# Kernel tuning notes

Hardware: AMD Instinct MI355X
Metric: run time of the kernel (lower is better)

Reference implementation:

```python
import jax, jax.numpy as jnp
import numpy as np

EMBED = 768
HEADS = 12
HEAD_DIM = EMBED // HEADS
WINDOW_SIZES = (16, 64, 256)
LN_EPS = 1e-5


def setup_inputs() -> dict:
    key = jax.random.key(0)
    ks = jax.random.split(key, 8)
    B, S = 4, 1024
    s = 1.0 / np.sqrt(EMBED)
    return {
        "query": jax.random.normal(ks[0], (B, S, EMBED), dtype=jnp.float32),
        "key": jax.random.normal(ks[1], (B, S, EMBED), dtype=jnp.float32),
        "value": jax.random.normal(ks[2], (B, S, EMBED), dtype=jnp.float32),
        "attention_mask": jnp.ones((B, S), dtype=jnp.float32),
        "Wq": jax.random.normal(ks[3], (EMBED, EMBED), dtype=jnp.float32) * s,
        "bq": jnp.zeros((EMBED,), dtype=jnp.float32),
        "Wk": jax.random.normal(ks[4], (EMBED, EMBED), dtype=jnp.float32) * s,
        "bk": jnp.zeros((EMBED,), dtype=jnp.float32),
        "Wv": jax.random.normal(ks[5], (EMBED, EMBED), dtype=jnp.float32) * s,
        "bv": jnp.zeros((EMBED,), dtype=jnp.float32),
        "window_weights": jnp.ones((len(WINDOW_SIZES),), dtype=jnp.float32) / len(WINDOW_SIZES),
        "gamma": jnp.ones((EMBED,), dtype=jnp.float32),
        "beta": jnp.zeros((EMBED,), dtype=jnp.float32),
    }


def reference(query, key, value, attention_mask, Wq, bq, Wk, bk, Wv, bv,
              window_weights, gamma, beta):
    B, S, _ = query.shape

    def proj(x, W, b):
        # [B,S,E] -> [B,H,S,D]  (torch nn.Linear: x @ W.T + b)
        return (x @ W.T + b).reshape(B, S, HEADS, HEAD_DIM).transpose(0, 2, 1, 3)

    q = proj(query, Wq, bq)
    k = proj(key, Wk, bk)
    v = proj(value, Wv, bv)

    # full [B,H,S,S] scores (dropout in eval mode = identity)
    scores = jnp.einsum("bhqd,bhkd->bhqk", q, k) / np.sqrt(HEAD_DIM)

    idx = jnp.arange(S)
    am = attention_mask[:, None, None, :]  # broadcast over heads and query dim
    combined = jnp.zeros_like(scores)
    for i, w in enumerate(WINDOW_SIZES):
        # band mask |i-j| <= w; note scores are multiplicatively masked
        # and carried across scales, exactly as in the torch loop
        band = (jnp.abs(idx[:, None] - idx[None, :]) <= w).astype(scores.dtype)
        scores = scores * band * am
        combined = combined + window_weights[i] * jax.nn.softmax(scores, axis=-1)

    context = jnp.einsum("bhqk,bhkd->bhqd", combined, v)
    context = context.transpose(0, 2, 1, 3).reshape(B, S, EMBED)
    q_flat = q.transpose(0, 2, 1, 3).reshape(B, S, EMBED)

    x = q_flat + context
    mean = jnp.mean(x, axis=-1, keepdims=True)
    var = jnp.var(x, axis=-1, keepdims=True)
    return gamma * (x - mean) / jnp.sqrt(var + LN_EPS) + beta
```

## Files before the change

### kernel.cpp

```cpp
#include <hip/hip_runtime.h>
#include <hip/hip_bf16.h>

#define EMB   768
#define SEQ   1024
#define NBAT  4
#define MROWS 4096
#define NHEAD 12
#define HD    64
#define WIN   16
#define QB    16
#define KB    64
#define LN_EPS 1e-5f

typedef __attribute__((ext_vector_type(8))) short bf16x8;
typedef __attribute__((ext_vector_type(4))) float f32x4;
typedef unsigned short u16;
typedef unsigned int   u32;

static __device__ inline u16 f2bf(float f) {
    union { float f; u32 u; } a; a.f = f;
    u32 u = a.u;
    u32 r = (u + 0x7fffu + ((u >> 16) & 1u)) >> 16;
    return (u16)r;
}
static __device__ inline float bf2f(u16 x) {
    union { u32 u; float f; } c; c.u = ((u32)x) << 16; return c.f;
}

#define ACT4 786432u
#define WT4  147456u
__global__ __launch_bounds__(256) void cast_all(
    const float* __restrict__ q, const float* __restrict__ k, const float* __restrict__ v,
    const float* __restrict__ wq, const float* __restrict__ wk, const float* __restrict__ wv,
    u16* __restrict__ Abf, u16* __restrict__ Wbf, float* __restrict__ Vsum)
{
    u32 u = blockIdx.x * 256u + threadIdx.x;
    if (u < NBAT * EMB) Vsum[u] = 0.f;
    const float* src; u16* dst; u32 off;
    if (u < 3u * ACT4) {
        u32 which = u / ACT4;
        off = (u - which * ACT4) * 4u;
        src = which == 0 ? q : (which == 1 ? k : v);
        dst = Abf + (size_t)which * 3145728u + off;
    } else {
        u32 w2 = u - 3u * ACT4;
        u32 which = w2 / WT4;
        off = (w2 - which * WT4) * 4u;
        src = which == 0 ? wq : (which == 1 ? wk : wv);
        dst = Wbf + (size_t)which * 589824u + off;
    }
    float4 val = *(const float4*)(src + off);
    ushort4 o;
    o.x = f2bf(val.x); o.y = f2bf(val.y); o.z = f2bf(val.z); o.w = f2bf(val.w);
    *(ushort4*)dst = o;
}

#define GK 768
#define GN 768

static __device__ inline void gload_lds16(const void* g, void* l) {
    __builtin_amdgcn_global_load_lds((const __attribute__((address_space(1))) void*)g,
                                     (__attribute__((address_space(3))) void*)l, 16, 0, 0);
}

__global__ __launch_bounds__(256) void gemm_qkv(
    const u16* __restrict__ Abase, const u16* __restrict__ Wbase,
    const float* __restrict__ bq, const float* __restrict__ bk, const float* __restrict__ bv,
    u16* __restrict__ Qb, u16* __restrict__ Kb, u16* __restrict__ Vb,
    float* __restrict__ Vsum)
{
    const int z = blockIdx.z;
    const u16* A = Abase + (size_t)z * (MROWS * GK);
    const u16* W = Wbase + (size_t)z * (GN * GK);
    const float* bias = (z == 0) ? bq : ((z == 1) ? bk : bv);
    u16* Ob = (z == 0) ? Qb : ((z == 1) ? Kb : Vb);

    int id = blockIdx.y * 6 + blockIdx.x;
    int swz = (id & 7) * 48 + (id >> 3);
    const int bm = (swz / 6) * 64, bn = (swz % 6) * 128;

    const int tid = threadIdx.x, wave = tid >> 6, lane = tid & 63;

    __shared__ __align__(16) u16 As[2][64 * 64];
    __shared__ __align__(16) u16 Bs[2][128 * 64];

    f32x4 acc[2][4];
#pragma unroll
    for (int i = 0; i < 2; ++i)
#pragma unroll
        for (int j = 0; j < 4; ++j) acc[i][j] = (f32x4){0.f, 0.f, 0.f, 0.f};

    const int wr = (wave >> 1) * 32, wc = (wave & 1) * 64;
    const int r0 = lane & 15, hk = lane >> 4;

    int arow[2], acol[2], brow[4], bcol[4];
#pragma unroll
    for (int j = 0; j < 2; ++j) {
        int c = j * 256 + tid;
        arow[j] = c >> 3;
        acol[j] = ((c & 7) ^ (arow[j] & 7)) * 8;
    }
#pragma unroll
    for (int j = 0; j < 4; ++j) {
        int c = j * 256 + tid;
        brow[j] = c >> 3;
        bcol[j] = ((c & 7) ^ (brow[j] & 7)) * 8;
    }

#define GEMM_STAGE(buf, K0) do { \
    _Pragma("unroll") for (int j = 0; j < 2; ++j) \
        gload_lds16(A + (size_t)(bm + arow[j]) * GK + (K0) + acol[j], \
                    &As[buf][(j * 256 + tid) * 8]); \
    _Pragma("unroll") for (int j = 0; j < 4; ++j) \
        gload_lds16(W + (size_t)(bn + brow[j]) * GK + (K0) + bcol[j], \
                    &Bs[buf][(j * 256 + tid) * 8]); \
} while (0)

#define GEMM_COMPUTE(buf) do { \
    bf16x8 af[2][2], bg[2][4]; \
    _Pragma("unroll") for (int kk = 0; kk < 2; ++kk) { \
        _Pragma("unroll") for (int i = 0; i < 2; ++i) { \
            int ra = wr + i * 16 + r0; int sa = (kk * 4 + hk) ^ (ra & 7); \
            af[kk][i] = *(const bf16x8*)&As[buf][ra * 64 + sa * 8]; } \
        _Pragma("unroll") for (int j = 0; j < 4; ++j) { \
            int rb = wc + j * 16 + r0; int sb = (kk * 4 + hk) ^ (rb & 7); \
            bg[kk][j] = *(const bf16x8*)&Bs[buf][rb * 64 + sb * 8]; } } \
    _Pragma("unroll") for (int kk = 0; kk < 2; ++kk) \
    _Pragma("unroll") for (int i = 0; i < 2; ++i) \
    _Pragma("unroll") for (int j = 0; j < 4; ++j) \
        acc[i][j] = __builtin_amdgcn_mfma_f32_16x16x32_bf16(af[kk][i], bg[kk][j], acc[i][j], 0, 0, 0); \
} while (0)

    GEMM_STAGE(0, 0);
    for (int t = 0; t < 11; ++t) {
        int cur = t & 1;
        GEMM_STAGE(cur ^ 1, (t + 1) * 64);
        asm volatile("s_waitcnt vmcnt(6)" ::: "memory");
        __builtin_amdgcn_sched_barrier(0);
        __builtin_amdgcn_s_barrier();
        __builtin_amdgcn_sched_barrier(0);
        GEMM_COMPUTE(cur);
        __builtin_amdgcn_sched_barrier(0);
        __builtin_amdgcn_s_barrier();
        __builtin_amdgcn_sched_barrier(0);
    }
    asm volatile("s_waitcnt vmcnt(0)" ::: "memory");
    __builtin_amdgcn_sched_barrier(0);
    __builtin_amdgcn_s_barrier();
    __builtin_amdgcn_sched_barrier(0);
    GEMM_COMPUTE(1);

#undef GEMM_STAGE
#undef GEMM_COMPUTE

    const int cl = lane & 15, rb4 = (lane >> 4) * 4;
#pragma unroll
    for (int i = 0; i < 2; ++i)
#pragma unroll
        for (int j = 0; j < 4; ++j) {
            int col = bn + wc + j * 16 + cl;
            float b_ = bias[col];
#pragma unroll
            for (int r = 0; r < 4; ++r) {
                int row = bm + wr + i * 16 + rb4 + r;
                Ob[(size_t)row * GN + col] = f2bf(acc[i][j][r] + b_);
            }
        }

    if (z == 2) {
        const int bb = bm >> 10;
#pragma unroll
        for (int j = 0; j < 4; ++j) {
            int col = bn + wc + j * 16 + cl;
            float s = bias[col] * 8.f;
#pragma unroll
            for (int i = 0; i < 2; ++i)
#pragma unroll
                for (int r = 0; r < 4; ++r) s += acc[i][j][r];
            s += __shfl_xor(s, 16, 64);
            s += __shfl_xor(s, 32, 64);
            if (hk == 0)
                atomicAdd(&Vsum[bb * EMB + col], s);
        }
    }
}

__global__ __launch_bounds__(768, 3) void attn_ln(
    const u16* __restrict__ Qb, const u16* __restrict__ Kb, const u16* __restrict__ Vb,
    const float* __restrict__ Vsum, const float* __restrict__ am, const float* __restrict__ ww,
    const float* __restrict__ gamma, const float* __restrict__ beta, float* __restrict__ out)
{
    int id = blockIdx.x + 64 * blockIdx.y;
    int swz = (id & 7) * 32 + (id >> 3);
    const int qt = swz & 63, b = swz >> 6;

    const int q0 = qt * QB;
    int kstart = q0 - WIN;
    if (kstart < 0) kstart = 0;
    if (kstart > SEQ - KB) kstart = SEQ - KB;

    const int h = threadIdx.x >> 6, lane = threadIdx.x & 63;
    const int fr = lane & 15, hk = lane >> 4;
    const int kof = hk * 8, rowg = hk * 4;

    __shared__ __align__(16) u16 Ps[NHEAD][QB][68];
    __shared__ __align__(16) float xs[QB][772];
    __shared__ float ps1[QB][13], ps2[QB][13];
    __shared__ float mu[QB], rs[QB];

    const float w0 = ww[0], w1 = ww[1], w2 = ww[2];

    bf16x8 aq[2], bk4[4][2], bv4[4][2];
    {
        const u16* qb = Qb + ((size_t)(b * SEQ + q0)) * EMB + h * HD;
#pragma unroll
        for (int kk = 0; kk < 2; ++kk)
            aq[kk] = *(const bf16x8*)(qb + (size_t)fr * EMB + kk * 32 + kof);
        const u16* kb = Kb + ((size_t)(b * SEQ + kstart)) * EMB + h * HD;
#pragma unroll
        for (int nj = 0; nj < 4; ++nj)
#pragma unroll
            for (int kk = 0; kk < 2; ++kk)
                bk4[nj][kk] = *(const bf16x8*)(kb + (size_t)(nj * 16 + fr) * EMB + kk * 32 + kof);
        const u16* vb = Vb + ((size_t)(b * SEQ + kstart)) * EMB + h * HD;
#pragma unroll
        for (int nj = 0; nj < 4; ++nj)
#pragma unroll
            for (int kk = 0; kk < 2; ++kk) {
                union { bf16x8 v; u16 s[8]; } tmp;
#pragma unroll
                for (int j = 0; j < 8; ++j)
                    tmp.s[j] = vb[(size_t)(kk * 32 + kof + j) * EMB + nj * 16 + fr];
                bv4[nj][kk] = tmp.v;
            }
    }

    f32x4 sc[4];
#pragma unroll
    for (int j = 0; j < 4; ++j) sc[j] = (f32x4){0.f, 0.f, 0.f, 0.f};
#pragma unroll
    for (int kk = 0; kk < 2; ++kk)
#pragma unroll
        for (int nj = 0; nj < 4; ++nj)
            sc[nj] = __builtin_amdgcn_mfma_f32_16x16x32_bf16(aq[kk], bk4[nj][kk], sc[nj], 0, 0, 0);

    float amv[4];
#pragma unroll
    for (int nj = 0; nj < 4; ++nj) amv[nj] = am[b * SEQ + kstart + nj * 16 + fr];

    float t[4][4], cj[4][4], ua[4];
#pragma unroll
    for (int nj = 0; nj < 4; ++nj)
#pragma unroll
        for (int r = 0; r < 4; ++r) {
            int qrow = q0 + rowg + r;
            int kcol = kstart + nj * 16 + fr;
            int d = qrow - kcol; if (d < 0) d = -d;
            t[nj][r] = (d <= WIN) ? sc[nj][r] * 0.125f * amv[nj] : 0.f;
            cj[nj][r] = 0.f;
        }
#pragma unroll
    for (int r = 0; r < 4; ++r) ua[r] = 0.f;

#pragma unroll
    for (int it = 0; it < 3; ++it) {
        float wwi = it == 0 ? w0 : (it == 1 ? w1 : w2);
#pragma unroll
        for (int r = 0; r < 4; ++r) {
            float m = 0.f;
#pragma unroll
            for (int nj = 0; nj < 4; ++nj) m = fmaxf(m, t[nj][r]);
#pragma unroll
            for (int o = 1; o < 16; o <<= 1) m = fmaxf(m, __shfl_xor(m, o, 64));
            float e4[4], s = 0.f;
#pragma unroll
            for (int nj = 0; nj < 4; ++nj) { e4[nj] = __expf(t[nj][r] - m); s += e4[nj]; }
#pragma unroll
            for (int o = 1; o < 16; o <<= 1) s += __shfl_xor(s, o, 64);
            float un = __expf(-m);
            s += (float)(SEQ - KB) * un;
            float inv = wwi / s;
#pragma unroll
            for (int nj = 0; nj < 4; ++nj) cj[nj][r] += e4[nj] * inv;
            ua[r] += un * inv;
        }
        if (it < 2) {
#pragma unroll
            for (int nj = 0; nj < 4; ++nj)
#pragma unroll
                for (int r = 0; r < 4; ++r) t[nj][r] *= amv[nj];
        }
    }

#pragma unroll
    for (int nj = 0; nj < 4; ++nj)
#pragma unroll
        for (int r = 0; r < 4; ++r)
            Ps[h][rowg + r][nj * 16 + fr] = f2bf(cj[nj][r] - ua[r]);

    f32x4 pv[4];
#pragma unroll
    for (int j = 0; j < 4; ++j) pv[j] = (f32x4){0.f, 0.f, 0.f, 0.f};
#pragma unroll
    for (int kk = 0; kk < 2; ++kk) {
        bf16x8 ap = *(const bf16x8*)&Ps[h][fr][kk * 32 + kof];
#pragma unroll
        for (int nj = 0; nj < 4; ++nj)
            pv[nj] = __builtin_amdgcn_mfma_f32_16x16x32_bf16(ap, bv4[nj][kk], pv[nj], 0, 0, 0);
    }

    float vs[4];
#pragma unroll
    for (int nj = 0; nj < 4; ++nj) vs[nj] = Vsum[b * EMB + h * HD + nj * 16 + fr];

    float xv[4][4];
#pragma unroll
    for (int nj = 0; nj < 4; ++nj)
#pragma unroll
        for (int r = 0; r < 4; ++r) {
            int row = q0 + rowg + r;
            float qres = bf2f(Qb[((size_t)(b * SEQ + row)) * EMB + h * HD + nj * 16 + fr]);
            xv[nj][r] = qres + pv[nj][r] + ua[r] * vs[nj];
            xs[rowg + r][h * HD + nj * 16 + fr] = xv[nj][r];
        }

    float s1r[4], s2r[4];
#pragma unroll
    for (int r = 0; r < 4; ++r) {
        float a = 0.f, c = 0.f;
#pragma unroll
        for (int nj = 0; nj < 4; ++nj) { a += xv[nj][r]; c += xv[nj][r] * xv[nj][r]; }
#pragma unroll
        for (int o = 1; o < 16; o <<= 1) { a += __shfl_xor(a, o, 64); c += __shfl_xor(c, o, 64); }
        s1r[r] = a; s2r[r] = c;
    }
    if (fr == 0) {
#pragma unroll
        for (int r = 0; r < 4; ++r) { ps1[rowg + r][h] = s1r[r]; ps2[rowg + r][h] = s2r[r]; }
    }
    __syncthreads();
    if (h == 0 && lane < QB) {
        float a = 0.f, c = 0.f;
#pragma unroll
        for (int w = 0; w < NHEAD; ++w) { a += ps1[lane][w]; c += ps2[lane][w]; }
        float mean = a * (1.f / EMB);
        float var = c * (1.f / EMB) - mean * mean;
        mu[lane] = mean;
        rs[lane] = rsqrtf(var + LN_EPS);
    }
    __syncthreads();

    {
        const int tt = threadIdx.x;
        const int rbase = tt / 192, c4 = tt % 192;
        float4 g4 = *(const float4*)(gamma + c4 * 4);
        float4 b4 = *(const float4*)(beta + c4 * 4);
#pragma unroll
        for (int k4 = 0; k4 < 4; ++k4) {
            int row = rbase + k4 * 4;
            float4 x4 = *(const float4*)&xs[row][c4 * 4];
            float m_ = mu[row], r_ = rs[row];
            float4 o;
            o.x = g4.x * (x4.x - m_) * r_ + b4.x;
            o.y = g4.y * (x4.y - m_) * r_ + b4.y;
            o.z = g4.z * (x4.z - m_) * r_ + b4.z;
            o.w = g4.w * (x4.w - m_) * r_ + b4.w;
            *(float4*)(out + ((size_t)(b * SEQ + q0 + row)) * EMB + c4 * 4) = o;
        }
    }
}

extern "C" void kernel_launch(void* const* d_in, const int* in_sizes, int n_in,
                              void* d_out, int out_size, void* d_ws, size_t ws_size,
                              hipStream_t stream)
{
    const float* q     = (const float*)d_in[0];
    const float* k     = (const float*)d_in[1];
    const float* v     = (const float*)d_in[2];
    const float* amask = (const float*)d_in[3];
    const float* Wq    = (const float*)d_in[4];
    const float* bq    = (const float*)d_in[5];
    const float* Wk    = (const float*)d_in[6];
    const float* bk    = (const float*)d_in[7];
    const float* Wv    = (const float*)d_in[8];
    const float* bv    = (const float*)d_in[9];
    const float* ww    = (const float*)d_in[10];
    const float* gamma = (const float*)d_in[11];
    const float* beta  = (const float*)d_in[12];
    float* out = (float*)d_out;

    char* ws = (char*)d_ws;
    u16*   Abf  = (u16*)(ws);
    u16*   Wbf  = (u16*)(ws + 18874368);
    u16*   Qbf  = (u16*)(ws + 22413312);
    u16*   Kbf  = (u16*)(ws + 28704768);
    u16*   Vbf  = (u16*)(ws + 34996224);
    float* Vsum = (float*)(ws + 41287680);

    hipLaunchKernelGGL(cast_all, dim3(10944), dim3(256), 0, stream,
                       q, k, v, Wq, Wk, Wv, Abf, Wbf, Vsum);
    hipLaunchKernelGGL(gemm_qkv, dim3(GN / 128, MROWS / 64, 3), dim3(256), 0, stream,
                       Abf, Wbf, bq, bk, bv, Qbf, Kbf, Vbf, Vsum);
    hipLaunchKernelGGL(attn_ln, dim3(SEQ / QB, NBAT), dim3(768), 0, stream,
                       Qbf, Kbf, Vbf, Vsum, amask, ww, gamma, beta, out);
}
```

Before: 56.54 us.

## Fuse fp32-to-bf16 activation cast into the QKV GEMM A-tile loading

Removes the separate cast of query/key/value activations to bf16. The GEMM now loads fp32 A tiles straight into registers, converts them and writes bf16 into swizzled LDS, double-buffered across iterations. The cast kernel now only converts the weights. This avoids writing and re-reading about 18 MB of bf16 activations, at the cost of more register pressure and extra VALU and LDS-store work inside the GEMM loop. Each A tile is now re-read from global memory in fp32 by every N-block.

Result: slower. 60.92 us (+7.8%).

```diff
diff --git a/kernel.cpp b/kernel.cpp
--- a/kernel.cpp
+++ b/kernel.cpp
@@ -26,33 +26,31 @@
 static __device__ inline float bf2f(u16 x) {
     union { u32 u; float f; } c; c.u = ((u32)x) << 16; return c.f;
 }
-
-#define ACT4 786432u
+static __device__ inline u32 cvt2(float lo, float hi) {
+    __hip_bfloat162 t = __float22bfloat162_rn(float2{lo, hi});
+    union { __hip_bfloat162 h; u32 u; } c; c.h = t; return c.u;
+}
+static __device__ inline bf16x8 pack8(float4 a, float4 b) {
+    union { bf16x8 v; u32 w[4]; } r;
+    r.w[0] = cvt2(a.x, a.y); r.w[1] = cvt2(a.z, a.w);
+    r.w[2] = cvt2(b.x, b.y); r.w[3] = cvt2(b.z, b.w);
+    return r.v;
+}
+
 #define WT4  147456u
-__global__ __launch_bounds__(256) void cast_all(
-    const float* __restrict__ q, const float* __restrict__ k, const float* __restrict__ v,
+__global__ __launch_bounds__(256) void cast_w(
     const float* __restrict__ wq, const float* __restrict__ wk, const float* __restrict__ wv,
-    u16* __restrict__ Abf, u16* __restrict__ Wbf, float* __restrict__ Vsum)
+    u16* __restrict__ Wbf, float* __restrict__ Vsum)
 {
     u32 u = blockIdx.x * 256u + threadIdx.x;
     if (u < NBAT * EMB) Vsum[u] = 0.f;
-    const float* src; u16* dst; u32 off;
-    if (u < 3u * ACT4) {
-        u32 which = u / ACT4;
-        off = (u - which * ACT4) * 4u;
-        src = which == 0 ? q : (which == 1 ? k : v);
-        dst = Abf + (size_t)which * 3145728u + off;
-    } else {
-        u32 w2 = u - 3u * ACT4;
-        u32 which = w2 / WT4;
-        off = (w2 - which * WT4) * 4u;
-        src = which == 0 ? wq : (which == 1 ? wk : wv);
-        dst = Wbf + (size_t)which * 589824u + off;
-    }
+    u32 which = u / WT4;
+    u32 off = (u - which * WT4) * 4u;
+    const float* src = which == 0 ? wq : (which == 1 ? wk : wv);
     float4 val = *(const float4*)(src + off);
     ushort4 o;
     o.x = f2bf(val.x); o.y = f2bf(val.y); o.z = f2bf(val.z); o.w = f2bf(val.w);
-    *(ushort4*)dst = o;
+    *(ushort4*)(Wbf + (size_t)which * 589824u + off) = o;
 }
 
 #define GK 768
@@ -64,13 +62,14 @@
 }
 
 __global__ __launch_bounds__(256) void gemm_qkv(
-    const u16* __restrict__ Abase, const u16* __restrict__ Wbase,
+    const float* __restrict__ qa, const float* __restrict__ ka, const float* __restrict__ va,
+    const u16* __restrict__ Wbase,
     const float* __restrict__ bq, const float* __restrict__ bk, const float* __restrict__ bv,
     u16* __restrict__ Qb, u16* __restrict__ Kb, u16* __restrict__ Vb,
     float* __restrict__ Vsum)
 {
     const int z = blockIdx.z;
-    const u16* A = Abase + (size_t)z * (MROWS * GK);
+    const float* Af = (z == 0) ? qa : ((z == 1) ? ka : va);
     const u16* W = Wbase + (size_t)z * (GN * GK);
     const float* bias = (z == 0) ? bq : ((z == 1) ? bk : bv);
     u16* Ob = (z == 0) ? Qb : ((z == 1) ? Kb : Vb);
@@ -93,13 +92,12 @@
     const int wr = (wave >> 1) * 32, wc = (wave & 1) * 64;
     const int r0 = lane & 15, hk = lane >> 4;
 
-    int arow[2], acol[2], brow[4], bcol[4];
-#pragma unroll
-    for (int j = 0; j < 2; ++j) {
-        int c = j * 256 + tid;
-        arow[j] = c >> 3;
-        acol[j] = ((c & 7) ^ (arow[j] & 7)) * 8;
-    }
+    const int ar = tid >> 2, ac2 = (tid & 3) * 2;
+    const float* arowp = Af + (size_t)(bm + ar) * GK + (tid & 3) * 16;
+    const int asw0 = ar * 64 + ((ac2 ^ (ar & 7)) * 8);
+    const int asw1 = ar * 64 + (((ac2 + 1) ^ (ar & 7)) * 8);
+
+    int brow[4], bcol[4];
 #pragma unroll
     for (int j = 0; j < 4; ++j) {
         int c = j * 256 + tid;
@@ -107,14 +105,28 @@
         bcol[j] = ((c & 7) ^ (brow[j] & 7)) * 8;
     }
 
-#define GEMM_STAGE(buf, K0) do { \
-    _Pragma("unroll") for (int j = 0; j < 2; ++j) \
-        gload_lds16(A + (size_t)(bm + arow[j]) * GK + (K0) + acol[j], \
-                    &As[buf][(j * 256 + tid) * 8]); \
+    float4 ae0, ae1, ae2, ae3;
+    float4 ao0, ao1, ao2, ao3;
+
+#define STAGE_W(buf, K0) do { \
     _Pragma("unroll") for (int j = 0; j < 4; ++j) \
         gload_lds16(W + (size_t)(bn + brow[j]) * GK + (K0) + bcol[j], \
                     &Bs[buf][(j * 256 + tid) * 8]); \
 } while (0)
+
+#define ALOAD_E(K0) do { const float* p = arowp + (K0); \
+    ae0 = *(const float4*)p; ae1 = *(const float4*)(p + 4); \
+    ae2 = *(const float4*)(p + 8); ae3 = *(const float4*)(p + 12); } while (0)
+#define ALOAD_O(K0) do { const float* p = arowp + (K0); \
+    ao0 = *(const float4*)p; ao1 = *(const float4*)(p + 4); \
+    ao2 = *(const float4*)(p + 8); ao3 = *(const float4*)(p + 12); } while (0)
+
+#define ACVT_E(buf) do { \
+    *(bf16x8*)&As[buf][asw0] = pack8(ae0, ae1); \
+    *(bf16x8*)&As[buf][asw1] = pack8(ae2, ae3); } while (0)
+#define ACVT_O(buf) do { \
+    *(bf16x8*)&As[buf][asw0] = pack8(ao0, ao1); \
+    *(bf16x8*)&As[buf][asw1] = pack8(ao2, ao3); } while (0)
 
 #define GEMM_COMPUTE(buf) do { \
     bf16x8 af[2][2], bg[2][4]; \
@@ -131,11 +143,22 @@
         acc[i][j] = __builtin_amdgcn_mfma_f32_16x16x32_bf16(af[kk][i], bg[kk][j], acc[i][j], 0, 0, 0); \
 } while (0)
 
-    GEMM_STAGE(0, 0);
-    for (int t = 0; t < 11; ++t) {
+    STAGE_W(0, 0);
+    __builtin_amdgcn_sched_barrier(0);
+    ALOAD_E(0);
+    __builtin_amdgcn_sched_barrier(0);
+
+    for (int t = 0; t < 12; ++t) {
         int cur = t & 1;
-        GEMM_STAGE(cur ^ 1, (t + 1) * 64);
-        asm volatile("s_waitcnt vmcnt(6)" ::: "memory");
+        if (t < 11) {
+            STAGE_W(cur ^ 1, (t + 1) * 64);
+            __builtin_amdgcn_sched_barrier(0);
+            if (cur == 0) ALOAD_O((t + 1) * 64);
+            else          ALOAD_E((t + 1) * 64);
+            __builtin_amdgcn_sched_barrier(0);
+        }
+        if (cur == 0) ACVT_E(0); else ACVT_O(1);
+        asm volatile("s_waitcnt lgkmcnt(0)" ::: "memory");
         __builtin_amdgcn_sched_barrier(0);
         __builtin_amdgcn_s_barrier();
         __builtin_amdgcn_sched_barrier(0);
@@ -144,13 +167,12 @@
         __builtin_amdgcn_s_barrier();
         __builtin_amdgcn_sched_barrier(0);
     }
-    asm volatile("s_waitcnt vmcnt(0)" ::: "memory");
-    __builtin_amdgcn_sched_barrier(0);
-    __builtin_amdgcn_s_barrier();
-    __builtin_amdgcn_sched_barrier(0);
-    GEMM_COMPUTE(1);
-
-#undef GEMM_STAGE
+
+#undef STAGE_W
+#undef ALOAD_E
+#undef ALOAD_O
+#undef ACVT_E
+#undef ACVT_O
 #undef GEMM_COMPUTE
 
     const int cl = lane & 15, rb4 = (lane >> 4) * 4;
@@ -390,17 +412,16 @@
     float* out = (float*)d_out;
 
     char* ws = (char*)d_ws;
-    u16*   Abf  = (u16*)(ws);
-    u16*   Wbf  = (u16*)(ws + 18874368);
-    u16*   Qbf  = (u16*)(ws + 22413312);
-    u16*   Kbf  = (u16*)(ws + 28704768);
-    u16*   Vbf  = (u16*)(ws + 34996224);
-    float* Vsum = (float*)(ws + 41287680);
-
-    hipLaunchKernelGGL(cast_all, dim3(10944), dim3(256), 0, stream,
-                       q, k, v, Wq, Wk, Wv, Abf, Wbf, Vsum);
+    u16*   Wbf  = (u16*)(ws);
+    u16*   Qbf  = (u16*)(ws + 3538944);
+    u16*   Kbf  = (u16*)(ws + 9830400);
+    u16*   Vbf  = (u16*)(ws + 16121856);
+    float* Vsum = (float*)(ws + 22413312);
+
+    hipLaunchKernelGGL(cast_w, dim3(1728), dim3(256), 0, stream,
+                       Wq, Wk, Wv, Wbf, Vsum);
     hipLaunchKernelGGL(gemm_qkv, dim3(GN / 128, MROWS / 64, 3), dim3(256), 0, stream,
-                       Abf, Wbf, bq, bk, bv, Qbf, Kbf, Vbf, Vsum);
+                       q, k, v, Wbf, bq, bk, bv, Qbf, Kbf, Vbf, Vsum);
     hipLaunchKernelGGL(attn_ln, dim3(SEQ / QB, NBAT), dim3(768), 0, stream,
                        Qbf, Kbf, Vbf, Vsum, amask, ww, gamma, beta, out);
 }
```
